# Kernel optimization log

Hardware: AMD Instinct MI355X
Metric: run time of the kernel (lower is better)

Reference implementation:

```python
import jax, jax.numpy as jnp
import numpy as np

ROUTING_ITERATIONS = 3


def squash(x):
    # x: [..., d]
    s2 = jnp.sum(x * x, axis=-1, keepdims=True)
    return x * (s2 / (1.0 + s2)) / jnp.sqrt(s2)


def setup_inputs() -> dict:
    key = jax.random.key(0)
    k1, k2 = jax.random.split(key)
    B, P, J, Dp, D = 16, 1024, 32, 64, 64
    inp = jax.random.normal(k1, (B, P, Dp), dtype=jnp.float32)
    # RandomUniform(-0.05, 0.05) initializer in the original
    W = jax.random.uniform(k2, (1, P, J, Dp, D), dtype=jnp.float32, minval=-0.05, maxval=0.05)
    b = jnp.zeros((1, P, J, D), dtype=jnp.float32)
    return {"inp": inp, "W": W, "b": b}


def reference(inp, W, b):
    B, P, Dp = inp.shape
    J = W.shape[2]
    # predictions u_hat: [B, P, J, D] via per-(p,j) Dp x D matmul
    u = jnp.einsum('bpe,pjed->bpjd', inp, W[0]) + b
    u_sg = jax.lax.stop_gradient(u)
    bij = jnp.zeros((B, P, J), dtype=inp.dtype)
    vj = None
    for it in range(ROUTING_ITERATIONS):
        cij = jax.nn.softmax(bij, axis=-1)[..., None]  # [B,P,J,1]
        if it == ROUTING_ITERATIONS - 1:
            vj = jnp.sum(cij * u, axis=1)  # [B,J,D]
            vj = squash(vj)  # squash_last=True
        else:
            vj = squash(jnp.sum(cij * u_sg, axis=1))  # [B,J,D]
            bij = bij + jnp.sum(vj[:, None] * u_sg, axis=-1)  # agreement [B,P,J]
    return vj
```

## Files before the change

kernel.cpp:

```cpp
#include <hip/hip_runtime.h>
#include <math.h>

#define B_  16
#define P_  1024
#define J_  32
#define D_  64
#define DP_ 64

typedef float v4 __attribute__((ext_vector_type(4)));

__global__ __launch_bounds__(256, 2) void k_umat(const float* __restrict__ x,
                                                 const float* __restrict__ W,
                                                 const float* __restrict__ bias,
                                                 float* __restrict__ u) {
  const int p  = blockIdx.x;
  const int t  = threadIdx.x;
  const int jg = t >> 4;
  const int d0 = (t & 15) << 2;

  __shared__ float sx[64 * 17];
  {
    const int e = t & 63, b4 = t >> 6;
#pragma unroll
    for (int i = 0; i < 4; ++i) {
      const int b = b4 * 4 + i;
      sx[e * 17 + b] = x[(size_t)(b * P_ + p) * DP_ + e];
    }
  }
  __syncthreads();

  const float* Wp = W + (size_t)p * (J_ * DP_ * D_);
  const float* bp = bias + (size_t)p * (J_ * D_);

  v4 acc0[16], acc1[16];
  const v4 bv0 = *(const v4*)&bp[jg * D_ + d0];
  const v4 bv1 = *(const v4*)&bp[(jg + 16) * D_ + d0];
#pragma unroll
  for (int b = 0; b < 16; ++b) { acc0[b] = bv0; acc1[b] = bv1; }

  const float* w0 = Wp + (size_t)jg * (DP_ * D_) + d0;
  const float* w1 = Wp + (size_t)(jg + 16) * (DP_ * D_) + d0;

#pragma unroll 2
  for (int e = 0; e < 64; ++e) {
    const v4 wa = *(const v4*)&w0[e * D_];
    const v4 wb = *(const v4*)&w1[e * D_];
#pragma unroll
    for (int b = 0; b < 16; ++b) {
      const float xv = sx[e * 17 + b];
      acc0[b] += wa * xv;
      acc1[b] += wb * xv;
    }
  }

#pragma unroll
  for (int b = 0; b < 16; ++b) {
    const size_t base = (size_t)(b * P_ + p) * (J_ * D_);
    *(v4*)&u[base + jg * D_ + d0]        = acc0[b];
    *(v4*)&u[base + (jg + 16) * D_ + d0] = acc1[b];
  }
}

__global__ __launch_bounds__(256) void k_mean_squash(const float* __restrict__ u,
                                                     float* __restrict__ vj) {
  const int b = blockIdx.x >> 5, j = blockIdx.x & 31;
  const int t = threadIdx.x;
  const int d0 = (t & 15) << 2, pg = t >> 4;

  v4 s = {0.f, 0.f, 0.f, 0.f};
  for (int p = pg; p < P_; p += 16)
    s += *(const v4*)&u[((size_t)(b * P_ + p) * J_ + j) * D_ + d0];

  __shared__ __align__(16) float sred[16][64];
  *(v4*)&sred[pg][d0] = s;
  __syncthreads();

  if (t < 64) {
    float v = 0.f;
#pragma unroll
    for (int g = 0; g < 16; ++g) v += sred[g][t];
    v *= (1.0f / 32.0f);
    float s2 = v * v;
#pragma unroll
    for (int o = 32; o; o >>= 1) s2 += __shfl_xor(s2, o);
    const float f = sqrtf(s2) / (1.0f + s2);
    vj[(size_t)blockIdx.x * D_ + t] = v * f;
  }
}

template <int FIRST>
__global__ __launch_bounds__(256) void k_route(const float* __restrict__ u,
                                               const float* __restrict__ vj,
                                               float* __restrict__ bij,
                                               float* __restrict__ part) {
  const int b = blockIdx.x >> 6, pb = blockIdx.x & 63;
  const int t = threadIdx.x;
  const int jg = t >> 4, d0 = (t & 15) << 2;
  const int j0 = jg, j1 = jg + 16;

  __shared__ __align__(16) float svj[J_ * D_];
  __shared__ float sag[32];
  __shared__ float sc[2][32];

  for (int i = t; i < J_ * D_; i += 256) svj[i] = vj[b * (J_ * D_) + i];
  __syncthreads();

  const v4 vv0 = *(const v4*)&svj[j0 * D_ + d0];
  const v4 vv1 = *(const v4*)&svj[j1 * D_ + d0];
  v4 acc0 = {0.f, 0.f, 0.f, 0.f}, acc1 = {0.f, 0.f, 0.f, 0.f};

  for (int pi = 0; pi < 16; ++pi) {
    const int p = pb * 16 + pi;
    const size_t ub = (size_t)(b * P_ + p) * (J_ * D_);
    const v4 u0 = *(const v4*)&u[ub + j0 * D_ + d0];
    const v4 u1 = *(const v4*)&u[ub + j1 * D_ + d0];

    float bold = 0.f;
    if (!FIRST && t < 32) bold = bij[(size_t)(b * P_ + p) * J_ + t];

    const v4 q0 = u0 * vv0, q1 = u1 * vv1;
    float a0 = q0[0] + q0[1] + q0[2] + q0[3];
    float a1 = q1[0] + q1[1] + q1[2] + q1[3];
#pragma unroll
    for (int o = 8; o; o >>= 1) {
      a0 += __shfl_xor(a0, o);
      a1 += __shfl_xor(a1, o);
    }
    if ((t & 15) == 0) { sag[j0] = a0; sag[j1] = a1; }
    __syncthreads();

    if (t < 32) {
      const float bn = bold + sag[t];
      bij[(size_t)(b * P_ + p) * J_ + t] = bn;
      float m = bn;
#pragma unroll
      for (int o = 16; o; o >>= 1) m = fmaxf(m, __shfl_xor(m, o));
      const float e = __expf(bn - m);
      float sum = e;
#pragma unroll
      for (int o = 16; o; o >>= 1) sum += __shfl_xor(sum, o);
      sc[pi & 1][t] = e / sum;
    }
    __syncthreads();

    const float c0 = sc[pi & 1][j0];
    const float c1 = sc[pi & 1][j1];
    acc0 += u0 * c0;
    acc1 += u1 * c1;
  }

  const size_t pbase = (size_t)blockIdx.x * (J_ * D_);
  *(v4*)&part[pbase + j0 * D_ + d0] = acc0;
  *(v4*)&part[pbase + j1 * D_ + d0] = acc1;
}

__global__ __launch_bounds__(64) void k_red_squash(const float* __restrict__ part,
                                                   float* __restrict__ outp) {
  const int b = blockIdx.x >> 5, j = blockIdx.x & 31;
  const int d = threadIdx.x;
  float s = 0.f;
#pragma unroll 8
  for (int pb = 0; pb < 64; ++pb)
    s += part[(size_t)(b * 64 + pb) * (J_ * D_) + j * D_ + d];
  float s2 = s * s;
#pragma unroll
  for (int o = 32; o; o >>= 1) s2 += __shfl_xor(s2, o);
  const float f = sqrtf(s2) / (1.0f + s2);
  outp[(size_t)blockIdx.x * D_ + d] = s * f;
}

extern "C" void kernel_launch(void* const* d_in, const int* in_sizes, int n_in,
                              void* d_out, int out_size, void* d_ws, size_t ws_size,
                              hipStream_t stream) {
  const float* x    = (const float*)d_in[0];
  const float* W    = (const float*)d_in[1];
  const float* bias = (const float*)d_in[2];
  float* out = (float*)d_out;

  char* ws = (char*)d_ws;
  float* u    = (float*)(ws);
  float* bij  = (float*)(ws + (size_t)134217728);
  float* part = (float*)(ws + (size_t)134217728 + 2097152);
  float* vj0  = (float*)(ws + (size_t)134217728 + 2097152 + 8388608);
  float* vj1  = vj0 + (B_ * J_ * D_);

  k_umat<<<P_, 256, 0, stream>>>(x, W, bias, u);
  k_mean_squash<<<B_ * J_, 256, 0, stream>>>(u, vj0);
  k_route<1><<<B_ * 64, 256, 0, stream>>>(u, vj0, bij, part);
  k_red_squash<<<B_ * J_, 64, 0, stream>>>(part, vj1);
  k_route<0><<<B_ * 64, 256, 0, stream>>>(u, vj1, bij, part);
  k_red_squash<<<B_ * J_, 64, 0, stream>>>(part, out);
}
```

Baseline: 800.7 us.

## Make routing wave-local without block barriers and widen umat to 512 threads

The routing kernel now assigns each 64-lane wavefront 8 capsules and keeps all 32 output rows in registers. Agreement, softmax and the weighted accumulation are all done with shuffles, so the per-capsule __syncthreads and shared-memory round trips are gone. The u-prediction kernel uses 512 threads with one j row per thread and nontemporal W loads, trading fewer accumulators per thread for more parallelism. The partial-sum buffer doubles to 128 partials per batch, which adds work to the final reduction.

```diff
diff --git a/kernel.cpp b/kernel.cpp
--- a/kernel.cpp
+++ b/kernel.cpp
@@ -6,58 +6,52 @@
 #define J_  32
 #define D_  64
 #define DP_ 64
+#define TILE_ 2048
 
 typedef float v4 __attribute__((ext_vector_type(4)));
 
-__global__ __launch_bounds__(256, 2) void k_umat(const float* __restrict__ x,
+__device__ __forceinline__ v4 ntload4(const float* p) {
+  return __builtin_nontemporal_load((const v4*)p);
+}
+
+__global__ __launch_bounds__(512, 4) void k_umat(const float* __restrict__ x,
                                                  const float* __restrict__ W,
                                                  const float* __restrict__ bias,
                                                  float* __restrict__ u) {
   const int p  = blockIdx.x;
   const int t  = threadIdx.x;
-  const int jg = t >> 4;
+  const int j  = t >> 4;
   const int d0 = (t & 15) << 2;
 
-  __shared__ float sx[64 * 17];
+  __shared__ float sx[64][17];
   {
-    const int e = t & 63, b4 = t >> 6;
+    const int i = t;
 #pragma unroll
-    for (int i = 0; i < 4; ++i) {
-      const int b = b4 * 4 + i;
-      sx[e * 17 + b] = x[(size_t)(b * P_ + p) * DP_ + e];
+    for (int it = 0; it < 2; ++it) {
+      const int idx = i + it * 512;
+      const int b = idx >> 6, e = idx & 63;
+      sx[e][b] = x[(size_t)(b * P_ + p) * DP_ + e];
     }
   }
   __syncthreads();
 
-  const float* Wp = W + (size_t)p * (J_ * DP_ * D_);
-  const float* bp = bias + (size_t)p * (J_ * D_);
+  const float* wp = W + (size_t)p * (J_ * DP_ * D_) + (size_t)j * (DP_ * D_) + d0;
+  const v4 bv = *(const v4*)&bias[(size_t)p * (J_ * D_) + j * D_ + d0];
 
-  v4 acc0[16], acc1[16];
-  const v4 bv0 = *(const v4*)&bp[jg * D_ + d0];
-  const v4 bv1 = *(const v4*)&bp[(jg + 16) * D_ + d0];
+  v4 acc[16];
 #pragma unroll
-  for (int b = 0; b < 16; ++b) { acc0[b] = bv0; acc1[b] = bv1; }
+  for (int b = 0; b < 16; ++b) acc[b] = bv;
 
-  const float* w0 = Wp + (size_t)jg * (DP_ * D_) + d0;
-  const float* w1 = Wp + (size_t)(jg + 16) * (DP_ * D_) + d0;
-
-#pragma unroll 2
+#pragma unroll 4
   for (int e = 0; e < 64; ++e) {
-    const v4 wa = *(const v4*)&w0[e * D_];
-    const v4 wb = *(const v4*)&w1[e * D_];
+    const v4 w = ntload4(wp + e * D_);
 #pragma unroll
-    for (int b = 0; b < 16; ++b) {
-      const float xv = sx[e * 17 + b];
-      acc0[b] += wa * xv;
-      acc1[b] += wb * xv;
-    }
+    for (int b = 0; b < 16; ++b) acc[b] += w * sx[e][b];
   }
 
 #pragma unroll
   for (int b = 0; b < 16; ++b) {
-    const size_t base = (size_t)(b * P_ + p) * (J_ * D_);
-    *(v4*)&u[base + jg * D_ + d0]        = acc0[b];
-    *(v4*)&u[base + (jg + 16) * D_ + d0] = acc1[b];
+    *(v4*)&u[(size_t)(b * P_ + p) * TILE_ + j * D_ + d0] = acc[b];
   }
 }
 
@@ -69,7 +63,7 @@
 
   v4 s = {0.f, 0.f, 0.f, 0.f};
   for (int p = pg; p < P_; p += 16)
-    s += *(const v4*)&u[((size_t)(b * P_ + p) * J_ + j) * D_ + d0];
+    s += *(const v4*)&u[(size_t)(b * P_ + p) * TILE_ + j * D_ + d0];
 
   __shared__ __align__(16) float sred[16][64];
   *(v4*)&sred[pg][d0] = s;
@@ -93,65 +87,76 @@
                                                const float* __restrict__ vj,
                                                float* __restrict__ bij,
                                                float* __restrict__ part) {
-  const int b = blockIdx.x >> 6, pb = blockIdx.x & 63;
-  const int t = threadIdx.x;
-  const int jg = t >> 4, d0 = (t & 15) << 2;
-  const int j0 = jg, j1 = jg + 16;
+  const int b     = blockIdx.x >> 5;
+  const int chunk = blockIdx.x & 31;
+  const int w     = threadIdx.x >> 6;
+  const int l     = threadIdx.x & 63;
+  const int l4    = l >> 4;
+  const int lq    = l & 15;
+  const int pw    = chunk * 4 + w;
+  const int p0    = pw * 8;
 
-  __shared__ __align__(16) float svj[J_ * D_];
-  __shared__ float sag[32];
-  __shared__ float sc[2][32];
+  const v4* vjv = (const v4*)(vj + (size_t)b * TILE_);
+  v4 vv[8];
+#pragma unroll
+  for (int k = 0; k < 8; ++k) vv[k] = vjv[(4 * k + l4) * 16 + lq];
 
-  for (int i = t; i < J_ * D_; i += 256) svj[i] = vj[b * (J_ * D_) + i];
-  __syncthreads();
+  v4 acc[8];
+#pragma unroll
+  for (int k = 0; k < 8; ++k) acc[k] = (v4){0.f, 0.f, 0.f, 0.f};
 
-  const v4 vv0 = *(const v4*)&svj[j0 * D_ + d0];
-  const v4 vv1 = *(const v4*)&svj[j1 * D_ + d0];
-  v4 acc0 = {0.f, 0.f, 0.f, 0.f}, acc1 = {0.f, 0.f, 0.f, 0.f};
+  for (int pi = 0; pi < 8; ++pi) {
+    const int p = p0 + pi;
+    const size_t bp = (size_t)(b * P_ + p);
+    const v4* up = (const v4*)(u + bp * TILE_);
 
-  for (int pi = 0; pi < 16; ++pi) {
-    const int p = pb * 16 + pi;
-    const size_t ub = (size_t)(b * P_ + p) * (J_ * D_);
-    const v4 u0 = *(const v4*)&u[ub + j0 * D_ + d0];
-    const v4 u1 = *(const v4*)&u[ub + j1 * D_ + d0];
+    v4 uf[8];
+#pragma unroll
+    for (int k = 0; k < 8; ++k) uf[k] = up[k * 64 + l];
 
-    float bold = 0.f;
-    if (!FIRST && t < 32) bold = bij[(size_t)(b * P_ + p) * J_ + t];
+    float a[8];
+#pragma unroll
+    for (int k = 0; k < 8; ++k) {
+      const v4 q = uf[k] * vv[k];
+      a[k] = (q[0] + q[1]) + (q[2] + q[3]);
+    }
+#pragma unroll
+    for (int o = 1; o <= 8; o <<= 1) {
+#pragma unroll
+      for (int k = 0; k < 8; ++k) a[k] += __shfl_xor(a[k], o);
+    }
 
-    const v4 q0 = u0 * vv0, q1 = u1 * vv1;
-    float a0 = q0[0] + q0[1] + q0[2] + q0[3];
-    float a1 = q1[0] + q1[1] + q1[2] + q1[3];
+    float bn[8];
+    if (FIRST) {
 #pragma unroll
-    for (int o = 8; o; o >>= 1) {
-      a0 += __shfl_xor(a0, o);
-      a1 += __shfl_xor(a1, o);
+      for (int k = 0; k < 8; ++k) bn[k] = a[k];
+      if (lq == 0) {
+#pragma unroll
+        for (int k = 0; k < 8; ++k) bij[bp * J_ + 4 * k + l4] = bn[k];
+      }
+    } else {
+#pragma unroll
+      for (int k = 0; k < 8; ++k) bn[k] = a[k] + bij[bp * J_ + 4 * k + l4];
     }
-    if ((t & 15) == 0) { sag[j0] = a0; sag[j1] = a1; }
-    __syncthreads();
 
-    if (t < 32) {
-      const float bn = bold + sag[t];
-      bij[(size_t)(b * P_ + p) * J_ + t] = bn;
-      float m = bn;
+    float m = bn[0];
 #pragma unroll
-      for (int o = 16; o; o >>= 1) m = fmaxf(m, __shfl_xor(m, o));
-      const float e = __expf(bn - m);
-      float sum = e;
+    for (int k = 1; k < 8; ++k) m = fmaxf(m, bn[k]);
+    m = fmaxf(m, __shfl_xor(m, 16));
+    m = fmaxf(m, __shfl_xor(m, 32));
+    float ex[8], s = 0.f;
 #pragma unroll
-      for (int o = 16; o; o >>= 1) sum += __shfl_xor(sum, o);
-      sc[pi & 1][t] = e / sum;
-    }
-    __syncthreads();
-
-    const float c0 = sc[pi & 1][j0];
-    const float c1 = sc[pi & 1][j1];
-    acc0 += u0 * c0;
-    acc1 += u1 * c1;
+    for (int k = 0; k < 8; ++k) { ex[k] = __expf(bn[k] - m); s += ex[k]; }
+    s += __shfl_xor(s, 16);
+    s += __shfl_xor(s, 32);
+    const float inv = 1.0f / s;
+#pragma unroll
+    for (int k = 0; k < 8; ++k) acc[k] += uf[k] * (ex[k] * inv);
   }
 
-  const size_t pbase = (size_t)blockIdx.x * (J_ * D_);
-  *(v4*)&part[pbase + j0 * D_ + d0] = acc0;
-  *(v4*)&part[pbase + j1 * D_ + d0] = acc1;
+  v4* pp = (v4*)(part + (size_t)(b * 128 + pw) * TILE_);
+#pragma unroll
+  for (int k = 0; k < 8; ++k) pp[k * 64 + l] = acc[k];
 }
 
 __global__ __launch_bounds__(64) void k_red_squash(const float* __restrict__ part,
@@ -160,8 +165,8 @@
   const int d = threadIdx.x;
   float s = 0.f;
 #pragma unroll 8
-  for (int pb = 0; pb < 64; ++pb)
-    s += part[(size_t)(b * 64 + pb) * (J_ * D_) + j * D_ + d];
+  for (int pw = 0; pw < 128; ++pw)
+    s += part[(size_t)(b * 128 + pw) * TILE_ + j * D_ + d];
   float s2 = s * s;
 #pragma unroll
   for (int o = 32; o; o >>= 1) s2 += __shfl_xor(s2, o);
@@ -181,13 +186,13 @@
   float* u    = (float*)(ws);
   float* bij  = (float*)(ws + (size_t)134217728);
   float* part = (float*)(ws + (size_t)134217728 + 2097152);
-  float* vj0  = (float*)(ws + (size_t)134217728 + 2097152 + 8388608);
+  float* vj0  = (float*)(ws + (size_t)134217728 + 2097152 + 16777216);
   float* vj1  = vj0 + (B_ * J_ * D_);
 
-  k_umat<<<P_, 256, 0, stream>>>(x, W, bias, u);
+  k_umat<<<P_, 512, 0, stream>>>(x, W, bias, u);
   k_mean_squash<<<B_ * J_, 256, 0, stream>>>(u, vj0);
-  k_route<1><<<B_ * 64, 256, 0, stream>>>(u, vj0, bij, part);
+  k_route<1><<<512, 256, 0, stream>>>(u, vj0, bij, part);
   k_red_squash<<<B_ * J_, 64, 0, stream>>>(part, vj1);
-  k_route<0><<<B_ * 64, 256, 0, stream>>>(u, vj1, bij, part);
+  k_route<0><<<512, 256, 0, stream>>>(u, vj1, bij, part);
   k_red_squash<<<B_ * J_, 64, 0, stream>>>(part, out);
 }
```

Result: no change. 790.1 us (-1.3%).
